# Optimization experiments

Hardware: AMD Instinct MI355X
Metric: run time of the kernel (lower is better)

The kernel has to match this reference:

```python
import jax, jax.numpy as jnp
import numpy as np

B, N, F = 4, 1024, 256
AVG_DEG = 16.0


def setup_inputs() -> dict:
    key = jax.random.key(0)
    k1, k2, k3, k4 = jax.random.split(key, 4)
    u = jax.random.uniform(k1, (B, N, N))
    A = (u < AVG_DEG / N).astype(jnp.float32)
    A = jnp.maximum(A, jnp.swapaxes(A, 1, 2))            # symmetric
    A = A * (1.0 - jnp.eye(N, dtype=jnp.float32))        # no self loops (added in forward)
    x = jax.random.normal(k2, (B, N, F), dtype=jnp.float32)
    pos = jax.random.normal(k3, (B, N, 3), dtype=jnp.float32)
    order = jax.random.uniform(k4, (B, N), dtype=jnp.float32)  # 'random' ordering priorities
    node_mask = jnp.ones((B, N), dtype=bool)
    return {"x": x, "adj": A, "pos": pos, "order": order, "node_mask": node_mask}


def _select(order, excluded, included, node_mask):
    # Greedy frontier-based node selection (K-MIS with stride=2).
    Bn, Nn = order.shape
    ar = jnp.arange(Nn)
    idx0 = jnp.argmin(order, axis=-1).astype(jnp.int32)           # [B]
    available = node_mask
    frontier = ar[None, :] == idx0[:, None]                        # scatter idx0 -> True
    selected = jnp.zeros_like(available)

    def cond(st):
        av, fr, sel, idx = st
        return av.any()

    def body(st):
        av, fr, sel, idx = st
        current = ar[None, :] == idx[:, None]                      # [B,N] one-hot
        sel = sel | current
        exc_row = jnp.take_along_axis(excluded, idx[:, None, None], axis=1)[:, 0]  # excluded[current]
        inc_row = jnp.take_along_axis(included, idx[:, None, None], axis=1)[:, 0]  # included[current]
        av = av & ~current & ~exc_row
        fr = (fr | inc_row | ~fr.any(-1, keepdims=True)) & av      # restart frontier if empty
        mo = jnp.where(fr, order, jnp.inf)
        midx = jnp.argmin(mo, axis=-1).astype(jnp.int32)
        has_fr = fr.any(-1)
        idx = jnp.where(has_fr, midx, idx)
        return (av, fr, sel, idx)

    _, _, selected, _ = jax.lax.while_loop(cond, body, (available, frontier, selected, idx0))
    return selected


def _forward(x, adj, pos, order, node_mask):
    Nn = adj.shape[1]
    eye = jnp.eye(Nn, dtype=adj.dtype)
    adj1 = jnp.where(node_mask[:, :, None], adj + eye, 0.0)        # adj_k[1] = A + I, masked rows
    adj2 = adj1 @ adj                                              # adj_k[2] = (A+I) @ A
    excluded = adj1 != 0                                           # adj_k[stride-1].bool()
    included = adj2 != 0                                           # adj_k[stride].bool()
    selected = _select(jax.lax.stop_gradient(order), excluded, included, node_mask)
    # pad K to N instead of data-dependent num_nodes; mask zeroes the padding
    mask_f, perm = jax.lax.top_k(selected.astype(jnp.float32), Nn)  # [B,K], [B,K]
    adj_kernel = jnp.take_along_axis(adj1, perm[:, None, :], axis=2)  # [B,N,K]
    # add_pool: adj^T @ x, then mask
    x_p = jnp.einsum('bnk,bnf->bkf', adj_kernel, x) * mask_f[..., None]
    # mean_pool for pos: add_pool / column degree
    deg = adj_kernel.sum(axis=1)[..., None]                        # [B,K,1]
    pos_p = jnp.einsum('bnk,bnc->bkc', adj_kernel, pos) / deg * mask_f[..., None]
    # coarsened adjacency: gather cols then rows of adj_k[stride], mask both sides
    a = jnp.take_along_axis(adj2, perm[:, None, :], axis=2)
    a = jnp.take_along_axis(a, perm[:, :, None], axis=1)
    a = a * mask_f[:, None, :] * mask_f[:, :, None]
    return x_p, pos_p, a, mask_f.astype(bool)


def reference(x, adj, pos, order, node_mask):
    return _forward(x, adj, pos, order, node_mask)
```

## Files before the change

kernel.cpp:

```cpp
#include <hip/hip_runtime.h>
#include <hip/hip_bf16.h>

#define BB 4
#define NN 1024
#define FF 256
#define NBLK 1024
#define NTHR 256

typedef __hip_bfloat16 bf16;
typedef unsigned long long u64;
typedef unsigned int u32;
typedef unsigned short u16;
typedef unsigned char u8;

__device__ __forceinline__ bf16 f2b(float v) { return __float2bfloat16(v); }
__device__ __forceinline__ u16 f2bbits(float v) {
    bf16 h = __float2bfloat16(v);
    u16 s; __builtin_memcpy(&s, &h, 2);
    return s;
}
template <typename OT> __device__ __forceinline__ OT fromf(float v);
template <> __device__ __forceinline__ float fromf<float>(float v) { return v; }
template <> __device__ __forceinline__ bf16 fromf<bf16>(float v) { return __float2bfloat16(v); }

__device__ __forceinline__ void st_wt(u32* p, u32 v)   { __hip_atomic_store(p, v, __ATOMIC_RELAXED, __HIP_MEMORY_SCOPE_SYSTEM); }
__device__ __forceinline__ void st_wt(u64* p, u64 v)   { __hip_atomic_store(p, v, __ATOMIC_RELAXED, __HIP_MEMORY_SCOPE_SYSTEM); }
__device__ __forceinline__ void st_wt(int* p, int v)   { __hip_atomic_store(p, v, __ATOMIC_RELAXED, __HIP_MEMORY_SCOPE_SYSTEM); }
__device__ __forceinline__ void st_wt(float* p, float v){ __hip_atomic_store(p, v, __ATOMIC_RELAXED, __HIP_MEMORY_SCOPE_SYSTEM); }

__device__ __forceinline__ void grid_sync(int* bars, int phase) {
    __syncthreads();
    if (threadIdx.x == 0) {
        asm volatile("s_waitcnt vmcnt(0)" ::: "memory");
        int* gc = bars + 320 + ((blockIdx.x >> 4) << 5);
        int v = __hip_atomic_fetch_add(gc, 1, __ATOMIC_RELAXED, __HIP_MEMORY_SCOPE_AGENT);
        if (v == phase * 16 - 1) {
            int r = __hip_atomic_fetch_add(bars, 1, __ATOMIC_RELAXED, __HIP_MEMORY_SCOPE_AGENT);
            if (r == phase * 64 - 1)
                for (int xx = 0; xx < 8; xx++)
                    __hip_atomic_store(bars + 32 + 32 * xx, phase,
                                       __ATOMIC_RELAXED, __HIP_MEMORY_SCOPE_AGENT);
        }
        int* flag = bars + 32 + 32 * (blockIdx.x & 7);
        int spins = 0;
        while (__hip_atomic_load(flag, __ATOMIC_RELAXED, __HIP_MEMORY_SCOPE_AGENT) < phase) {
            if (spins < 16) __builtin_amdgcn_s_sleep(2);
            else            __builtin_amdgcn_s_sleep(32);
            if (++spins > (1 << 20)) break;
        }
        asm volatile("" ::: "memory");
    }
    __syncthreads();
}

template <typename OT>
__global__ __launch_bounds__(NTHR, 4) void mega_kernel(
        const float* __restrict__ x, const float* __restrict__ adj,
        const float* __restrict__ pos, const float* __restrict__ order,
        u64* __restrict__ bitsA, u32* __restrict__ packed,
        int* __restrict__ sp2node, int* __restrict__ node2sp,
        int* __restrict__ perm, int* __restrict__ kcnt,
        float* __restrict__ xpool, float* __restrict__ pospool,
        int* __restrict__ sink, int* __restrict__ bar,
        OT* __restrict__ out, size_t out_elems)
{
    const int B = blockIdx.x, t = threadIdx.x;
    __shared__ union ShU {
        u64 keys[NN];
        struct {
            u64 myrow[16], incw[16], part[256];
            int s2nT[16 * 65];
            u16 nbr[192];
            int cnt;
        } pb;
        struct {
            u64 myrow[16];
            u8 selS[NN];
            u16 nbr[192];
            int cnt;
        } pc;
        struct {
            int p[NN];
            u64 myrow[16];
            u16 sta[NN];
        } pd;
    } sh;

    for (int i = 0; i < 4; i++) {
        const int id = B * 4 + i;
        const int b = id >> 10, r = id & (NN - 1);
        const size_t base = (size_t)b * NN * NN + (size_t)r * NN;
        for (int q = 0; q < 4; q++) {
            int j = q * 256 + t;
            u64 bal = __ballot(adj[base + j] != 0.0f);
            if ((t & 63) == 0) st_wt(&bitsA[((size_t)b * NN + r) * 16 + (j >> 6)], bal);
        }
    }
    if (B < 8) {
        const int b = B >> 1, half = B & 1;
        for (int i = t; i < NN; i += NTHR) {
            float v = order[(size_t)b * NN + i];
            u32 ub = __float_as_uint(v);
            u32 sk = (ub & 0x80000000u) ? ~ub : (ub | 0x80000000u);
            sh.keys[i] = ((u64)sk << 32) | (u32)i;
        }
        __syncthreads();
        u64 mk0 = sh.keys[half * 512 + t], mk1 = sh.keys[half * 512 + 256 + t];
        int r0 = 0, r1 = 0;
        for (int m = 0; m < NN; m++) {
            u64 v = sh.keys[m];
            r0 += (v < mk0);
            r1 += (v < mk1);
        }
        int n0 = (int)(mk0 & 0xFFFFFFFFu), n1 = (int)(mk1 & 0xFFFFFFFFu);
        st_wt(&sp2node[b * NN + r0], n0); st_wt(&node2sp[b * NN + n0], r0);
        st_wt(&sp2node[b * NN + r1], n1); st_wt(&node2sp[b * NN + n1], r1);
    }
    grid_sync(bar, 1);

    {
        const int b = B >> 8, rbase = (B & 255) * 4;
        for (int q = 0; q < 4; q++) {
            int j = q * 256 + t;
            sh.pb.s2nT[(j & 15) * 65 + (j >> 4)] = sp2node[b * NN + j];
        }
        for (int rr = 0; rr < 4; rr++) {
            const int r = rbase + rr;
            if (t == 0) sh.pb.cnt = 0;
            if (t < 16) sh.pb.myrow[t] = bitsA[((size_t)b * NN + r) * 16 + t];
            __syncthreads();
            for (int q = 0; q < 4; q++) {
                int j = q * 256 + t;
                if ((sh.pb.myrow[j >> 6] >> (j & 63)) & 1) {
                    int p = atomicAdd(&sh.pb.cnt, 1);
                    if (p < 192) sh.pb.nbr[p] = (u16)j;
                }
            }
            __syncthreads();
            const int c = min(sh.pb.cnt, 192);
            {
                const int w = t & 15, g = t >> 4;
                u64 v = 0;
                for (int n = g; n < c; n += 16)
                    v |= bitsA[((size_t)b * NN + sh.pb.nbr[n]) * 16 + w];
                sh.pb.part[t] = v;
            }
            __syncthreads();
            if (t < 16) {
                u64 acc = sh.pb.myrow[t];
                for (int g = 0; g < 16; g++) acc |= sh.pb.part[g * 16 + t];
                sh.pb.incw[t] = acc;
            }
            __syncthreads();
            if (t < 64) {
                const int s = node2sp[b * NN + r];
                u32 e16 = 0, i16 = 0;
                for (int q = 0; q < 16; q++) {
                    int jn = sh.pb.s2nT[q * 65 + t];
                    u32 eb = (u32)((sh.pb.myrow[jn >> 6] >> (jn & 63)) & 1) | (u32)(jn == r);
                    u32 ib = (u32)((sh.pb.incw[jn >> 6] >> (jn & 63)) & 1);
                    e16 |= eb << q;
                    i16 |= ib << q;
                }
                st_wt(&packed[((size_t)b * NN + s) * 64 + t], e16 | (i16 << 16));
            }
            __syncthreads();
        }
    }
    grid_sync(bar, 2);

    if (B < 4) {
        const int b = B;
        const uint4* pp = (const uint4*)(packed + (size_t)b * NN * 64);
        u32 acc = 0;
        for (int i = t; i < NN * 16; i += NTHR) {
            uint4 v = pp[i];
            acc ^= v.x ^ v.y ^ v.z ^ v.w;
        }
        if (acc == 0xDEADBEEFu) atomicAdd(sink, 1);
        __syncthreads();

        if (t < 64) {
            const int l = t;
            u32 avail = 0xFFFFu, front = (l == 0) ? 1u : 0u, sel = 0u;
            int cur = 0;
            for (int iter = 0; iter < 2 * NN + 8; ++iter) {
                if ((cur >> 4) == l) sel |= 1u << (cur & 15);
                u32 p = packed[((size_t)b * NN + cur) * 64 + l];
                avail &= ~(p & 0xFFFFu);
                front = (front | (p >> 16)) & avail;
                u64 fb = __ballot(front != 0u);
                if (!fb) {
                    front = avail;
                    fb = __ballot(front != 0u);
                    if (!fb) break;
                }
                int lf = __ffsll(fb) - 1;
                u32 f = __shfl(front, lf);
                cur = lf * 16 + (__ffs(f) - 1);
            }
            for (int q = 0; q < 16; q++) sh.pc.selS[l * 16 + q] = (sel >> q) & 1u;
        }
        __syncthreads();
        if (t < 64) {
            const int l = t;
            u32 nodesel = 0;
            const int* n2s = node2sp + b * NN;
            for (int q = 0; q < 16; q++)
                nodesel |= ((u32)sh.pc.selS[n2s[l * 16 + q]]) << q;
            int cnt_sel = __popc(nodesel);
            int ps = cnt_sel;
            for (int off = 1; off < 64; off <<= 1) {
                int v = __shfl_up(ps, off);
                if (l >= off) ps += v;
            }
            const int K = __shfl(ps, 63);
            int pos_ = ps - cnt_sel;
            u32 m = nodesel;
            while (m) { int i = __ffs(m) - 1; st_wt(&perm[b * NN + pos_], l * 16 + i); pos_++; m &= m - 1; }
            int posu = K + l * 16 - (ps - cnt_sel);
            m = (~nodesel) & 0xFFFFu;
            while (m) { int i = __ffs(m) - 1; st_wt(&perm[b * NN + posu], l * 16 + i); posu++; m &= m - 1; }
            if (l == 0) st_wt(&kcnt[b], K);
        }
    } else {
        const size_t nb8 = (out_elems * sizeof(OT)) >> 3;
        u64* o8 = (u64*)out;
        for (size_t i = (size_t)(B - 4) * NTHR + t; i < nb8; i += (size_t)(NBLK - 4) * NTHR)
            st_wt(o8 + i, (u64)0);
        for (int task = B - 4; task < BB * NN; task += NBLK - 4) {
            const int b = task & 3, n = task >> 2;
            if (t == 0) sh.pc.cnt = 0;
            if (t < 16) sh.pc.myrow[t] = bitsA[((size_t)b * NN + n) * 16 + t];
            __syncthreads();
            for (int i = 0; i < 4; i++) {
                int j = i * 256 + t;
                if ((sh.pc.myrow[j >> 6] >> (j & 63)) & 1) {
                    int pp = atomicAdd(&sh.pc.cnt, 1);
                    if (pp < 192) sh.pc.nbr[pp] = (u16)j;
                }
            }
            __syncthreads();
            const int c = min(sh.pc.cnt, 192);
            const size_t xb = (size_t)b * NN * FF;
            float acc = x[xb + (size_t)n * FF + t];
            for (int i = 0; i < c; i++) acc += x[xb + (size_t)sh.pc.nbr[i] * FF + t];
            st_wt(&xpool[((size_t)b * NN + n) * FF + t], acc);
            if (t < 3) {
                const size_t pb_ = (size_t)b * NN * 3;
                float pa = pos[pb_ + n * 3 + t];
                for (int i = 0; i < c; i++) pa += pos[pb_ + sh.pc.nbr[i] * 3 + t];
                st_wt(&pospool[((size_t)b * NN + n) * 4 + t], pa / (float)(c + 1));
            }
            __syncthreads();
        }
    }
    grid_sync(bar, 3);

    OT* out_x = out;
    OT* out_pos = out_x + (size_t)BB * NN * FF;
    OT* out_a = out_pos + (size_t)BB * NN * 3;
    OT* out_mask = out_a + (size_t)BB * NN * NN;

    for (int task = B; task < BB * NN; task += NBLK) {
        const int b = task & 3, k = task >> 2;
        const int K = kcnt[b];
        if (k >= K) continue;
        const int r = perm[b * NN + k];
        OT* ox = out_x + ((size_t)b * NN + k) * FF;
        OT* op = out_pos + ((size_t)b * NN + k) * 3;
        OT* oa = out_a + ((size_t)b * NN + k) * NN;
        if (t == 0) out_mask[(size_t)b * NN + k] = fromf<OT>(1.0f);
        if (t < 16) sh.pd.myrow[t] = bitsA[((size_t)b * NN + r) * 16 + t];
        for (int q = 0; q < 4; q++) { int j = t + q * 256; sh.pd.p[j] = perm[b * NN + j]; }
        __syncthreads();

        if constexpr (sizeof(OT) == 2) {
            if (t < 32) {
                const float* xr = xpool + ((size_t)b * NN + r) * FF + t * 8;
                union { u16 w[8]; uint4 v; } u;
#pragma unroll
                for (int i = 0; i < 8; i++) u.w[i] = f2bbits(xr[i]);
                ((uint4*)ox)[t] = u.v;
            }
        } else {
            ox[t] = (OT)xpool[((size_t)b * NN + r) * FF + t];
        }
        if (t < 3) op[t] = fromf<OT>(pospool[((size_t)b * NN + r) * 4 + t]);

        if constexpr (sizeof(OT) == 2) {
            for (int q = 0; q < 4; q++) {
                int jj = t + q * 256;
                float v = 0.0f;
                if (jj < K) {
                    const int pj = sh.pd.p[jj];
                    const u64* rj = bitsA + ((size_t)b * NN + pj) * 16;
                    int a2 = (int)((sh.pd.myrow[pj >> 6] >> (pj & 63)) & 1);
#pragma unroll
                    for (int w = 0; w < 16; w++)
                        a2 += __popcll(sh.pd.myrow[w] & rj[w]);
                    v = (float)a2;
                }
                sh.pd.sta[jj] = f2bbits(v);
            }
            __syncthreads();
            const int nu = (K + 7) >> 3;
            if (t < nu) ((uint4*)oa)[t] = ((const uint4*)sh.pd.sta)[t];
            __syncthreads();
        } else {
            for (int q = 0; q < 4; q++) {
                int jj = t + q * 256;
                if (jj < K) {
                    const int pj = sh.pd.p[jj];
                    const u64* rj = bitsA + ((size_t)b * NN + pj) * 16;
                    int a2 = (int)((sh.pd.myrow[pj >> 6] >> (pj & 63)) & 1);
#pragma unroll
                    for (int w = 0; w < 16; w++)
                        a2 += __popcll(sh.pd.myrow[w] & rj[w]);
                    oa[jj] = (float)a2;
                }
            }
            __syncthreads();
        }
    }
}

extern "C" void kernel_launch(void* const* d_in, const int* in_sizes, int n_in,
                              void* d_out, int out_size, void* d_ws, size_t ws_size,
                              hipStream_t stream) {
    const float* x     = (const float*)d_in[0];
    const float* adj   = (const float*)d_in[1];
    const float* pos   = (const float*)d_in[2];
    const float* order = (const float*)d_in[3];

    char* ws = (char*)d_ws;
    size_t off = 0;
    u64* bitsA     = (u64*)(ws + off);  off += (size_t)BB * NN * 16 * 8;
    u32* packed    = (u32*)(ws + off);  off += (size_t)BB * NN * 64 * 4;
    int* sp2node   = (int*)(ws + off);  off += (size_t)BB * NN * 4;
    int* node2sp   = (int*)(ws + off);  off += (size_t)BB * NN * 4;
    int* perm      = (int*)(ws + off);  off += (size_t)BB * NN * 4;
    int* kcnt      = (int*)(ws + off);  off += 64;
    int* sink      = (int*)(ws + off);  off += 64;
    float* xpool   = (float*)(ws + off); off += (size_t)BB * NN * FF * 4;
    float* pospool = (float*)(ws + off); off += (size_t)BB * NN * 4 * 4;
    int* bar       = (int*)(ws + off);  off += 12288;

    hipMemsetAsync(bar, 0, 12288, stream);

    bool outf32 = false;
    size_t osz = 0;
    if (hipMemPtrGetInfo(d_out, &osz) == hipSuccess)
        outf32 = (osz >= 4ull * (size_t)out_size);

    if (outf32)
        mega_kernel<float><<<NBLK, NTHR, 0, stream>>>(x, adj, pos, order, bitsA, packed,
            sp2node, node2sp, perm, kcnt, xpool, pospool, sink, bar,
            (float*)d_out, (size_t)out_size);
    else
        mega_kernel<bf16><<<NBLK, NTHR, 0, stream>>>(x, adj, pos, order, bitsA, packed,
            sp2node, node2sp, perm, kcnt, xpool, pospool, sink, bar,
            (bf16*)d_out, (size_t)out_size);
}
```

Before: 154.5 us.

## Split grid into specialized block groups with partial barriers to overlap phases

The 1024 blocks are now split into three roles instead of running every phase across the whole grid. 512 blocks bitpack adjacency, build the packed matrix and run the serial selection. 504 blocks zero the output and pool x/pos straight from adj, overlapping with the selection. 8 blocks sort the order keys and signal completion with a counter. Three full grid barriers become two partial tree barriers plus one final grid barrier. Also added: neighbor lists built by a warp prefix scan instead of shared atomics, the first 128 packed rows staged in LDS for the serial loop, and an unrolled pooling gather. The risk is load imbalance between roles and extra redundant adj reads in the pooling blocks.

```diff
diff --git a/kernel.cpp b/kernel.cpp
--- a/kernel.cpp
+++ b/kernel.cpp
@@ -6,6 +6,10 @@
 #define FF 256
 #define NBLK 1024
 #define NTHR 256
+#define PBLK 512
+#define QN   504
+#define QPOOL 3584
+#define SROWS 128
 
 typedef __hip_bfloat16 bf16;
 typedef unsigned long long u64;
@@ -28,27 +32,77 @@
 __device__ __forceinline__ void st_wt(int* p, int v)   { __hip_atomic_store(p, v, __ATOMIC_RELAXED, __HIP_MEMORY_SCOPE_SYSTEM); }
 __device__ __forceinline__ void st_wt(float* p, float v){ __hip_atomic_store(p, v, __ATOMIC_RELAXED, __HIP_MEMORY_SCOPE_SYSTEM); }
 
-__device__ __forceinline__ void grid_sync(int* bars, int phase) {
+__device__ __forceinline__ void tree_sync(int* reg, int idx, int ngroups, int phase) {
     __syncthreads();
     if (threadIdx.x == 0) {
         asm volatile("s_waitcnt vmcnt(0)" ::: "memory");
-        int* gc = bars + 320 + ((blockIdx.x >> 4) << 5);
+        int* gc = reg + 32 * (9 + (idx >> 4));
         int v = __hip_atomic_fetch_add(gc, 1, __ATOMIC_RELAXED, __HIP_MEMORY_SCOPE_AGENT);
         if (v == phase * 16 - 1) {
-            int r = __hip_atomic_fetch_add(bars, 1, __ATOMIC_RELAXED, __HIP_MEMORY_SCOPE_AGENT);
-            if (r == phase * 64 - 1)
+            int r = __hip_atomic_fetch_add(reg, 1, __ATOMIC_RELAXED, __HIP_MEMORY_SCOPE_AGENT);
+            if (r == phase * ngroups - 1)
                 for (int xx = 0; xx < 8; xx++)
-                    __hip_atomic_store(bars + 32 + 32 * xx, phase,
+                    __hip_atomic_store(reg + 32 * (1 + xx), phase,
                                        __ATOMIC_RELAXED, __HIP_MEMORY_SCOPE_AGENT);
         }
-        int* flag = bars + 32 + 32 * (blockIdx.x & 7);
+        int* flag = reg + 32 * (1 + (idx & 7));
         int spins = 0;
         while (__hip_atomic_load(flag, __ATOMIC_RELAXED, __HIP_MEMORY_SCOPE_AGENT) < phase) {
-            if (spins < 16) __builtin_amdgcn_s_sleep(2);
-            else            __builtin_amdgcn_s_sleep(32);
+            if (spins < 64) __builtin_amdgcn_s_sleep(2);
+            else            __builtin_amdgcn_s_sleep(16);
             if (++spins > (1 << 20)) break;
         }
         asm volatile("" ::: "memory");
+    }
+    __syncthreads();
+}
+
+__device__ __forceinline__ int build_nbr(const u64* myrow, u16* nbr, int* cntp, int t) {
+    __syncthreads();
+    if (t < 16) {
+        int myc = __popcll(myrow[t]);
+        int ps = myc;
+#pragma unroll
+        for (int off = 1; off < 16; off <<= 1) {
+            int v = __shfl_up(ps, off);
+            if (t >= off) ps += v;
+        }
+        int idx = ps - myc;
+        u64 m = myrow[t];
+        while (m) {
+            int i = __ffsll(m) - 1;
+            if (idx < 192) nbr[idx] = (u16)(t * 64 + i);
+            idx++;
+            m &= m - 1;
+        }
+        if (t == 15) *cntp = ps;
+    }
+    __syncthreads();
+    return min(*cntp, 192);
+}
+
+__device__ __forceinline__ void pool_task(int b, int n,
+        const float* __restrict__ x, const float* __restrict__ pos,
+        const u64* myrow, u16* nbr, int* cntp,
+        float* __restrict__ xpool, float* __restrict__ pospool, int t) {
+    const int c = build_nbr(myrow, nbr, cntp, t);
+    const float* xr = x + (size_t)b * NN * FF;
+    float acc = xr[(size_t)n * FF + t];
+    int i = 0;
+    for (; i + 4 <= c; i += 4) {
+        float a0 = xr[(size_t)nbr[i + 0] * FF + t];
+        float a1 = xr[(size_t)nbr[i + 1] * FF + t];
+        float a2 = xr[(size_t)nbr[i + 2] * FF + t];
+        float a3 = xr[(size_t)nbr[i + 3] * FF + t];
+        acc += a0; acc += a1; acc += a2; acc += a3;
+    }
+    for (; i < c; i++) acc += xr[(size_t)nbr[i] * FF + t];
+    st_wt(&xpool[((size_t)b * NN + n) * FF + t], acc);
+    if (t < 3) {
+        const size_t pb_ = (size_t)b * NN * 3;
+        float pa = pos[pb_ + n * 3 + t];
+        for (int j = 0; j < c; j++) pa += pos[pb_ + nbr[j] * 3 + t];
+        st_wt(&pospool[((size_t)b * NN + n) * 4 + t], pa / (float)(c + 1));
     }
     __syncthreads();
 }
@@ -75,9 +129,12 @@
         } pb;
         struct {
             u64 myrow[16];
-            u8 selS[NN];
             u16 nbr[192];
             int cnt;
+        } pl;
+        struct {
+            u32 stage[SROWS * 64];
+            u8 selS[NN];
         } pc;
         struct {
             int p[NN];
@@ -86,63 +143,45 @@
         } pd;
     } sh;
 
-    for (int i = 0; i < 4; i++) {
-        const int id = B * 4 + i;
-        const int b = id >> 10, r = id & (NN - 1);
-        const size_t base = (size_t)b * NN * NN + (size_t)r * NN;
-        for (int q = 0; q < 4; q++) {
-            int j = q * 256 + t;
-            u64 bal = __ballot(adj[base + j] != 0.0f);
-            if ((t & 63) == 0) st_wt(&bitsA[((size_t)b * NN + r) * 16 + (j >> 6)], bal);
-        }
-    }
-    if (B < 8) {
-        const int b = B >> 1, half = B & 1;
-        for (int i = t; i < NN; i += NTHR) {
-            float v = order[(size_t)b * NN + i];
-            u32 ub = __float_as_uint(v);
-            u32 sk = (ub & 0x80000000u) ? ~ub : (ub | 0x80000000u);
-            sh.keys[i] = ((u64)sk << 32) | (u32)i;
+    int* Greg = bar;
+    int* Preg = bar + 32 * 73;
+    int* srt  = bar + 32 * 114;
+
+    if (B < PBLK) {
+        const int b = B >> 7, rbase = (B * 8) & (NN - 1);
+        for (int i = 0; i < 8; i++) {
+            const int r = rbase + i;
+            const size_t base = (size_t)b * NN * NN + (size_t)r * NN;
+            for (int q = 0; q < 4; q++) {
+                int j = q * 256 + t;
+                u64 bal = __ballot(adj[base + j] != 0.0f);
+                if ((t & 63) == 0) st_wt(&bitsA[((size_t)b * NN + r) * 16 + (j >> 6)], bal);
+            }
+        }
+        tree_sync(Preg, B, 32, 1);
+        if (t == 0) {
+            int spins = 0;
+            while (__hip_atomic_load(srt, __ATOMIC_RELAXED, __HIP_MEMORY_SCOPE_AGENT) < 8) {
+                __builtin_amdgcn_s_sleep(2);
+                if (++spins > (1 << 20)) break;
+            }
+            asm volatile("" ::: "memory");
         }
         __syncthreads();
-        u64 mk0 = sh.keys[half * 512 + t], mk1 = sh.keys[half * 512 + 256 + t];
-        int r0 = 0, r1 = 0;
-        for (int m = 0; m < NN; m++) {
-            u64 v = sh.keys[m];
-            r0 += (v < mk0);
-            r1 += (v < mk1);
-        }
-        int n0 = (int)(mk0 & 0xFFFFFFFFu), n1 = (int)(mk1 & 0xFFFFFFFFu);
-        st_wt(&sp2node[b * NN + r0], n0); st_wt(&node2sp[b * NN + n0], r0);
-        st_wt(&sp2node[b * NN + r1], n1); st_wt(&node2sp[b * NN + n1], r1);
-    }
-    grid_sync(bar, 1);
-
-    {
-        const int b = B >> 8, rbase = (B & 255) * 4;
+
         for (int q = 0; q < 4; q++) {
             int j = q * 256 + t;
             sh.pb.s2nT[(j & 15) * 65 + (j >> 4)] = sp2node[b * NN + j];
         }
-        for (int rr = 0; rr < 4; rr++) {
+        for (int rr = 0; rr < 8; rr++) {
             const int r = rbase + rr;
-            if (t == 0) sh.pb.cnt = 0;
             if (t < 16) sh.pb.myrow[t] = bitsA[((size_t)b * NN + r) * 16 + t];
-            __syncthreads();
-            for (int q = 0; q < 4; q++) {
-                int j = q * 256 + t;
-                if ((sh.pb.myrow[j >> 6] >> (j & 63)) & 1) {
-                    int p = atomicAdd(&sh.pb.cnt, 1);
-                    if (p < 192) sh.pb.nbr[p] = (u16)j;
-                }
-            }
-            __syncthreads();
-            const int c = min(sh.pb.cnt, 192);
+            const int c = build_nbr(sh.pb.myrow, sh.pb.nbr, &sh.pb.cnt, t);
             {
                 const int w = t & 15, g = t >> 4;
                 u64 v = 0;
-                for (int n = g; n < c; n += 16)
-                    v |= bitsA[((size_t)b * NN + sh.pb.nbr[n]) * 16 + w];
+                for (int n2 = g; n2 < c; n2 += 16)
+                    v |= bitsA[((size_t)b * NN + sh.pb.nbr[n2]) * 16 + w];
                 sh.pb.part[t] = v;
             }
             __syncthreads();
@@ -166,96 +205,115 @@
             }
             __syncthreads();
         }
-    }
-    grid_sync(bar, 2);
-
-    if (B < 4) {
-        const int b = B;
-        const uint4* pp = (const uint4*)(packed + (size_t)b * NN * 64);
-        u32 acc = 0;
-        for (int i = t; i < NN * 16; i += NTHR) {
-            uint4 v = pp[i];
-            acc ^= v.x ^ v.y ^ v.z ^ v.w;
-        }
-        if (acc == 0xDEADBEEFu) atomicAdd(sink, 1);
-        __syncthreads();
-
-        if (t < 64) {
-            const int l = t;
-            u32 avail = 0xFFFFu, front = (l == 0) ? 1u : 0u, sel = 0u;
-            int cur = 0;
-            for (int iter = 0; iter < 2 * NN + 8; ++iter) {
-                if ((cur >> 4) == l) sel |= 1u << (cur & 15);
-                u32 p = packed[((size_t)b * NN + cur) * 64 + l];
-                avail &= ~(p & 0xFFFFu);
-                front = (front | (p >> 16)) & avail;
-                u64 fb = __ballot(front != 0u);
-                if (!fb) {
-                    front = avail;
-                    fb = __ballot(front != 0u);
-                    if (!fb) break;
+        tree_sync(Preg, B, 32, 2);
+
+        if (B < 4) {
+            const int sb = B;
+            const u32* pk = packed + (size_t)sb * NN * 64;
+            u32 acc = 0;
+            for (int i = t; i < NN * 16; i += NTHR) {
+                uint4 v = ((const uint4*)pk)[i];
+                if ((i >> 4) < SROWS) ((uint4*)sh.pc.stage)[i] = v;
+                acc ^= v.x ^ v.y ^ v.z ^ v.w;
+            }
+            if (acc == 0xDEADBEEFu) atomicAdd(sink, 1);
+            __syncthreads();
+
+            if (t < 64) {
+                const int l = t;
+                u32 avail = 0xFFFFu, front = (l == 0) ? 1u : 0u, sel = 0u;
+                int cur = 0;
+                for (int iter = 0; iter < 2 * NN + 8; ++iter) {
+                    if ((cur >> 4) == l) sel |= 1u << (cur & 15);
+                    u32 p;
+                    if (cur < SROWS) p = sh.pc.stage[cur * 64 + l];
+                    else             p = pk[(size_t)cur * 64 + l];
+                    avail &= ~(p & 0xFFFFu);
+                    front = (front | (p >> 16)) & avail;
+                    u64 fb = __ballot(front != 0u);
+                    if (!fb) {
+                        front = avail;
+                        fb = __ballot(front != 0u);
+                        if (!fb) break;
+                    }
+                    int lf = __ffsll(fb) - 1;
+                    u32 f = (u32)__builtin_amdgcn_readlane((int)front, lf);
+                    cur = lf * 16 + (__ffs(f) - 1);
                 }
-                int lf = __ffsll(fb) - 1;
-                u32 f = __shfl(front, lf);
-                cur = lf * 16 + (__ffs(f) - 1);
-            }
-            for (int q = 0; q < 16; q++) sh.pc.selS[l * 16 + q] = (sel >> q) & 1u;
-        }
-        __syncthreads();
-        if (t < 64) {
-            const int l = t;
-            u32 nodesel = 0;
-            const int* n2s = node2sp + b * NN;
-            for (int q = 0; q < 16; q++)
-                nodesel |= ((u32)sh.pc.selS[n2s[l * 16 + q]]) << q;
-            int cnt_sel = __popc(nodesel);
-            int ps = cnt_sel;
-            for (int off = 1; off < 64; off <<= 1) {
-                int v = __shfl_up(ps, off);
-                if (l >= off) ps += v;
-            }
-            const int K = __shfl(ps, 63);
-            int pos_ = ps - cnt_sel;
-            u32 m = nodesel;
-            while (m) { int i = __ffs(m) - 1; st_wt(&perm[b * NN + pos_], l * 16 + i); pos_++; m &= m - 1; }
-            int posu = K + l * 16 - (ps - cnt_sel);
-            m = (~nodesel) & 0xFFFFu;
-            while (m) { int i = __ffs(m) - 1; st_wt(&perm[b * NN + posu], l * 16 + i); posu++; m &= m - 1; }
-            if (l == 0) st_wt(&kcnt[b], K);
-        }
-    } else {
+                for (int q = 0; q < 16; q++) sh.pc.selS[l * 16 + q] = (sel >> q) & 1u;
+            }
+            __syncthreads();
+            if (t < 64) {
+                const int l = t;
+                u32 nodesel = 0;
+                const int* n2s = node2sp + sb * NN;
+                for (int q = 0; q < 16; q++)
+                    nodesel |= ((u32)sh.pc.selS[n2s[l * 16 + q]]) << q;
+                int cnt_sel = __popc(nodesel);
+                int ps = cnt_sel;
+                for (int off = 1; off < 64; off <<= 1) {
+                    int v = __shfl_up(ps, off);
+                    if (l >= off) ps += v;
+                }
+                const int K = __shfl(ps, 63);
+                int pos_ = ps - cnt_sel;
+                u32 m = nodesel;
+                while (m) { int i = __ffs(m) - 1; st_wt(&perm[sb * NN + pos_], l * 16 + i); pos_++; m &= m - 1; }
+                int posu = K + l * 16 - (ps - cnt_sel);
+                m = (~nodesel) & 0xFFFFu;
+                while (m) { int i = __ffs(m) - 1; st_wt(&perm[sb * NN + posu], l * 16 + i); posu++; m &= m - 1; }
+                if (l == 0) st_wt(&kcnt[sb], K);
+            }
+        } else {
+            for (int task = QPOOL + (B - 4); task < BB * NN; task += PBLK - 4) {
+                const int tb = task & 3, n = task >> 2;
+                if (t < 16) sh.pl.myrow[t] = bitsA[((size_t)tb * NN + n) * 16 + t];
+                pool_task(tb, n, x, pos, sh.pl.myrow, sh.pl.nbr, &sh.pl.cnt,
+                          xpool, pospool, t);
+            }
+        }
+    } else if (B < PBLK + QN) {
+        const int zi = B - PBLK;
         const size_t nb8 = (out_elems * sizeof(OT)) >> 3;
         u64* o8 = (u64*)out;
-        for (size_t i = (size_t)(B - 4) * NTHR + t; i < nb8; i += (size_t)(NBLK - 4) * NTHR)
+        for (size_t i = (size_t)zi * NTHR + t; i < nb8; i += (size_t)QN * NTHR)
             st_wt(o8 + i, (u64)0);
-        for (int task = B - 4; task < BB * NN; task += NBLK - 4) {
-            const int b = task & 3, n = task >> 2;
-            if (t == 0) sh.pc.cnt = 0;
-            if (t < 16) sh.pc.myrow[t] = bitsA[((size_t)b * NN + n) * 16 + t];
-            __syncthreads();
-            for (int i = 0; i < 4; i++) {
-                int j = i * 256 + t;
-                if ((sh.pc.myrow[j >> 6] >> (j & 63)) & 1) {
-                    int pp = atomicAdd(&sh.pc.cnt, 1);
-                    if (pp < 192) sh.pc.nbr[pp] = (u16)j;
-                }
-            }
-            __syncthreads();
-            const int c = min(sh.pc.cnt, 192);
-            const size_t xb = (size_t)b * NN * FF;
-            float acc = x[xb + (size_t)n * FF + t];
-            for (int i = 0; i < c; i++) acc += x[xb + (size_t)sh.pc.nbr[i] * FF + t];
-            st_wt(&xpool[((size_t)b * NN + n) * FF + t], acc);
-            if (t < 3) {
-                const size_t pb_ = (size_t)b * NN * 3;
-                float pa = pos[pb_ + n * 3 + t];
-                for (int i = 0; i < c; i++) pa += pos[pb_ + sh.pc.nbr[i] * 3 + t];
-                st_wt(&pospool[((size_t)b * NN + n) * 4 + t], pa / (float)(c + 1));
-            }
-            __syncthreads();
-        }
-    }
-    grid_sync(bar, 3);
+        for (int task = zi; task < QPOOL; task += QN) {
+            const int tb = task & 3, n = task >> 2;
+            const size_t abase = (size_t)tb * NN * NN + (size_t)n * NN;
+            for (int q = 0; q < 4; q++) {
+                int j = q * 256 + t;
+                u64 bal = __ballot(adj[abase + j] != 0.0f);
+                if ((t & 63) == 0) sh.pl.myrow[j >> 6] = bal;
+            }
+            pool_task(tb, n, x, pos, sh.pl.myrow, sh.pl.nbr, &sh.pl.cnt,
+                      xpool, pospool, t);
+        }
+    } else {
+        const int b = (B - (PBLK + QN)) >> 1, half = (B - (PBLK + QN)) & 1;
+        for (int i = t; i < NN; i += NTHR) {
+            float v = order[(size_t)b * NN + i];
+            u32 ub = __float_as_uint(v);
+            u32 sk = (ub & 0x80000000u) ? ~ub : (ub | 0x80000000u);
+            sh.keys[i] = ((u64)sk << 32) | (u32)i;
+        }
+        __syncthreads();
+        u64 mk0 = sh.keys[half * 512 + t], mk1 = sh.keys[half * 512 + 256 + t];
+        int r0 = 0, r1 = 0;
+        for (int m = 0; m < NN; m++) {
+            u64 v = sh.keys[m];
+            r0 += (v < mk0);
+            r1 += (v < mk1);
+        }
+        int n0 = (int)(mk0 & 0xFFFFFFFFu), n1 = (int)(mk1 & 0xFFFFFFFFu);
+        st_wt(&sp2node[b * NN + r0], n0); st_wt(&node2sp[b * NN + n0], r0);
+        st_wt(&sp2node[b * NN + r1], n1); st_wt(&node2sp[b * NN + n1], r1);
+        __syncthreads();
+        if (t == 0)
+            __hip_atomic_fetch_add(srt, 1, __ATOMIC_RELAXED, __HIP_MEMORY_SCOPE_AGENT);
+    }
+
+    tree_sync(Greg, B, 64, 1);
 
     OT* out_x = out;
     OT* out_pos = out_x + (size_t)BB * NN * FF;
@@ -344,9 +402,9 @@
     int* sink      = (int*)(ws + off);  off += 64;
     float* xpool   = (float*)(ws + off); off += (size_t)BB * NN * FF * 4;
     float* pospool = (float*)(ws + off); off += (size_t)BB * NN * 4 * 4;
-    int* bar       = (int*)(ws + off);  off += 12288;
-
-    hipMemsetAsync(bar, 0, 12288, stream);
+    int* bar       = (int*)(ws + off);  off += 16384;
+
+    hipMemsetAsync(bar, 0, 16384, stream);
 
     bool outf32 = false;
     size_t osz = 0;
```

Result: slower. 158.3 us (+2.4%).
